# Optimization experiments

Hardware: AMD Instinct MI355X
Metric: run time of the kernel (lower is better)

The kernel has to match this reference:

```python
import jax, jax.numpy as jnp
import numpy as np
import math

MSG_K = 256  # min(active_count, 256); with uniform(0,1) activations active_count >> 256
N_HEADS = 4
LN_EPS = 1e-5


def _mha(x, wi, bi, wo, bo):
    # torch nn.MultiheadAttention self-attention, batch_first=True
    B, K, D = x.shape
    H = N_HEADS
    hd = D // H
    qkv = x @ wi.T + bi                      # [B,K,3D]
    q, k, v = jnp.split(qkv, 3, axis=-1)
    def split_heads(t):
        return t.reshape(B, K, H, hd).transpose(0, 2, 1, 3)  # [B,H,K,hd]
    q, k, v = split_heads(q), split_heads(k), split_heads(v)
    scores = jnp.einsum('bhqd,bhkd->bhqk', q, k) * (1.0 / math.sqrt(hd))
    attn = jax.nn.softmax(scores, axis=-1)
    o = jnp.einsum('bhqk,bhkd->bhqd', attn, v)
    o = o.transpose(0, 2, 1, 3).reshape(B, K, D)
    return o @ wo.T + bo


def _layernorm(x, g, b):
    mu = jnp.mean(x, axis=-1, keepdims=True)
    var = jnp.mean((x - mu) ** 2, axis=-1, keepdims=True)
    return (x - mu) * jax.lax.rsqrt(var + LN_EPS) * g + b


def setup_inputs() -> dict:
    key = jax.random.key(0)
    ks = jax.random.split(key, 12)
    B, N, D = 32, 4096, 256
    s = 0.02
    return {
        'activation': jax.random.uniform(ks[0], (B, N), dtype=jnp.float32),
        'hidden_state': jax.random.normal(ks[1], (B, N, D), dtype=jnp.float32),
        'in_proj_w': jax.random.normal(ks[2], (3 * D, D), dtype=jnp.float32) * s,
        'in_proj_b': jnp.zeros((3 * D,), jnp.float32),
        'out_proj_w': jax.random.normal(ks[3], (D, D), dtype=jnp.float32) * s,
        'out_proj_b': jnp.zeros((D,), jnp.float32),
        'su_w1': jax.random.normal(ks[4], (D, 2 * D), dtype=jnp.float32) * s,
        'su_b1': jnp.zeros((D,), jnp.float32),
        'su_w2': jax.random.normal(ks[5], (D, D), dtype=jnp.float32) * s,
        'su_b2': jnp.zeros((D,), jnp.float32),
        'au_w1': jax.random.normal(ks[6], (D, 2 * D), dtype=jnp.float32) * s,
        'au_b1': jnp.zeros((D,), jnp.float32),
        'au_w2': jax.random.normal(ks[7], (1, D), dtype=jnp.float32) * s,
        'au_b2': jnp.zeros((1,), jnp.float32),
        'ln_g': jnp.ones((D,), jnp.float32),
        'ln_b': jnp.zeros((D,), jnp.float32),
        'sparsity_k': 256,
    }


def reference(activation, hidden_state, in_proj_w, in_proj_b, out_proj_w, out_proj_b,
              su_w1, su_b1, su_w2, su_b2, au_w1, au_b1, au_w2, au_b2, ln_g, ln_b,
              sparsity_k):
    B, N, D = hidden_state.shape
    b_idx = jnp.arange(B)[:, None]

    # ---- compute_messages: top-k gather -> sparse MHA -> scatter back ----
    topk_vals, topk_idx = jax.lax.top_k(activation, MSG_K)        # [B,K]
    active_states = jnp.take_along_axis(hidden_state, topk_idx[..., None], axis=1)  # [B,K,D]
    msg_sparse = _mha(active_states, in_proj_w, in_proj_b, out_proj_w, out_proj_b)
    msg_sparse = msg_sparse * topk_vals[..., None]
    messages = jnp.zeros((B, N, D), hidden_state.dtype).at[b_idx, topk_idx].set(msg_sparse)

    # ---- update_states: MLP on [old, messages] + LayerNorm ----
    combined = jnp.concatenate([hidden_state, messages], axis=-1)  # [B,N,2D]
    h = jax.nn.gelu(combined @ su_w1.T + su_b1, approximate=False)
    new_hidden = _layernorm(h @ su_w2.T + su_b2, ln_g, ln_b)

    # ---- update_activations ----
    comb2 = jnp.concatenate([hidden_state, new_hidden], axis=-1)
    h2 = jax.nn.gelu(comb2 @ au_w1.T + au_b1, approximate=False)
    delta = jax.nn.sigmoid((h2 @ au_w2.T + au_b2).squeeze(-1))     # [B,N]
    new_activation = jnp.clip(0.7 * activation + 0.3 * delta, 0.0, 1.0)

    # ---- maintain_sparsity: keep top sparsity_k, zero the rest ----
    k = min(int(sparsity_k), N)
    tv, ti = jax.lax.top_k(new_activation, k)                      # [B,k]
    sparse_act = jnp.zeros_like(new_activation).at[b_idx, ti].set(tv)
    kept_hidden = jnp.take_along_axis(new_hidden, ti[..., None], axis=1)
    sparse_hidden = jnp.zeros_like(new_hidden).at[b_idx, ti].set(kept_hidden)
    return sparse_act, sparse_hidden
```

## Files before the change

kernel.cpp:

```cpp
#include <hip/hip_runtime.h>


constexpr int KC = 32;
constexpr int CMAX = 2304;
constexpr float BAND_EPS = 0.004f;
constexpr int MAXBAND = 512;

typedef short bf16x8 __attribute__((ext_vector_type(8)));
typedef float f32x4 __attribute__((ext_vector_type(4)));

__device__ __forceinline__ float gelu_f(float x) {
    return 0.5f * x * (1.0f + erff(x * 0.70710678118654752440f));
}
__device__ __forceinline__ unsigned short f2bf(float f) {
    unsigned u = __float_as_uint(f);
    return (unsigned short)((u + 0x7fffu + ((u >> 16) & 1u)) >> 16);
}
__device__ __forceinline__ float bf2f(unsigned short h) {
    return __uint_as_float(((unsigned)h) << 16);
}

__global__ void __launch_bounds__(256) fill0_k(float4* p, long n4) {
    long i = (long)blockIdx.x * 256 + threadIdx.x;
    long stride = (long)gridDim.x * 256;
    float4 z = make_float4(0.f, 0.f, 0.f, 0.f);
    for (; i < n4; i += stride) p[i] = z;
}

__global__ void __launch_bounds__(256) topk1_k(const float* __restrict__ act,
        float* __restrict__ svals, int* __restrict__ sidx, int* __restrict__ cnt)
{
    __shared__ int cs[4];
    __shared__ int sTop, sRest;
    int b = blockIdx.x, tid = threadIdx.x;
    int wid = tid >> 6, lane = tid & 63;
    unsigned v[16];
    #pragma unroll
    for (int s = 0; s < 16; ++s)
        v[s] = __float_as_uint(act[b * 4096 + s * 256 + tid]);

    auto reduce4 = [&](int c) -> int {
        #pragma unroll
        for (int off = 32; off >= 1; off >>= 1) c += __shfl_xor(c, off);
        if (lane == 0) cs[wid] = c;
        __syncthreads();
        int tot = cs[0] + cs[1] + cs[2] + cs[3];
        __syncthreads();
        return tot;
    };
    auto countGE = [&](unsigned thr) -> int {
        int c = 0;
        #pragma unroll
        for (int s = 0; s < 16; ++s) c += (v[s] >= thr) ? 1 : 0;
        return reduce4(c);
    };
    auto countEqLt = [&](unsigned vs, int icut) -> int {
        int c = 0;
        #pragma unroll
        for (int s = 0; s < 16; ++s)
            c += (v[s] == vs && (s * 256 + tid) < icut) ? 1 : 0;
        return reduce4(c);
    };

    unsigned vstar = 0;
    for (int bit = 31; bit >= 0; --bit) {
        unsigned cand = vstar | (1u << bit);
        if (countGE(cand) >= 256) vstar = cand;
    }
    int cgt = countGE(vstar + 1);
    int needed = 256 - cgt;
    int icut = 4096;
    if (countEqLt(vstar, 4096) > needed) {
        int lo = 0, hi = 4096;
        for (int it = 0; it < 12; ++it) {
            int mid = (lo + hi) >> 1;
            if (countEqLt(vstar, mid) <= needed) lo = mid; else hi = mid;
        }
        icut = lo;
    }
    if (tid == 0) { sTop = 0; sRest = 0; }
    __syncthreads();
    float th = __uint_as_float(vstar) - 0.4288f;
    #pragma unroll
    for (int s = 0; s < 16; ++s) {
        int i = s * 256 + tid;
        unsigned vb = v[s];
        float f = __uint_as_float(vb);
        bool top = (vb > vstar) || (vb == vstar && i < icut);
        if (top) {
            int slot = atomicAdd(&sTop, 1);
            sidx[b * 4096 + slot] = i;
            svals[b * 4096 + slot] = f;
        } else if (f >= th) {
            int slot = 256 + atomicAdd(&sRest, 1);
            if (slot < CMAX) {
                sidx[b * 4096 + slot] = i;
                svals[b * 4096 + slot] = f;
            }
        }
    }
    __syncthreads();
    if (tid == 0) cnt[b] = min(256 + sRest, CMAX);
}

__global__ void __launch_bounds__(256) topk2_k(const float* __restrict__ newact,
        const int* __restrict__ sidx, const int* __restrict__ cnt,
        float* __restrict__ selv, int* __restrict__ selo, int* __restrict__ selp)
{
    __shared__ int cs[4];
    __shared__ int sSel;
    int b = blockIdx.x, tid = threadIdx.x;
    int wid = tid >> 6, lane = tid & 63;
    int C = min(cnt[b], CMAX);
    unsigned v[9];
    int org[9];
    #pragma unroll
    for (int s = 0; s < 9; ++s) {
        int p = s * 256 + tid;
        bool ok = (p < C && p < CMAX);
        v[s] = ok ? __float_as_uint(newact[(long)b * CMAX + p]) : 0u;
        org[s] = ok ? sidx[b * 4096 + p] : 0x7FFFFFFF;
    }
    auto reduce4 = [&](int c) -> int {
        #pragma unroll
        for (int off = 32; off >= 1; off >>= 1) c += __shfl_xor(c, off);
        if (lane == 0) cs[wid] = c;
        __syncthreads();
        int tot = cs[0] + cs[1] + cs[2] + cs[3];
        __syncthreads();
        return tot;
    };
    auto countGE = [&](unsigned thr) -> int {
        int c = 0;
        #pragma unroll
        for (int s = 0; s < 9; ++s) c += (v[s] >= thr) ? 1 : 0;
        return reduce4(c);
    };
    auto countEqLt = [&](unsigned vs, int icut) -> int {
        int c = 0;
        #pragma unroll
        for (int s = 0; s < 9; ++s) c += (v[s] == vs && org[s] < icut) ? 1 : 0;
        return reduce4(c);
    };

    unsigned vstar = 0;
    for (int bit = 31; bit >= 0; --bit) {
        unsigned cand = vstar | (1u << bit);
        if (countGE(cand) >= 256) vstar = cand;
    }
    int cgt = countGE(vstar + 1);
    int needed = 256 - cgt;
    int icut = 4096;
    if (countEqLt(vstar, 4096) > needed) {
        int lo = 0, hi = 4096;
        for (int it = 0; it < 12; ++it) {
            int mid = (lo + hi) >> 1;
            if (countEqLt(vstar, mid) <= needed) lo = mid; else hi = mid;
        }
        icut = lo;
    }
    if (tid == 0) sSel = 0;
    __syncthreads();
    #pragma unroll
    for (int s = 0; s < 9; ++s) {
        unsigned vb = v[s];
        bool sel = (vb > vstar) || (vb == vstar && org[s] < icut);
        if (sel) {
            int slot = atomicAdd(&sSel, 1);
            selv[b * 256 + slot] = __uint_as_float(vb);
            selo[b * 256 + slot] = org[s];
            selp[b * 256 + slot] = s * 256 + tid;
        }
    }
}

template<int TM, int TN, int RM, int RN, bool BT, bool GATHER, int EPI>
__global__ void __launch_bounds__(256) gemm_k(
    const float* __restrict__ A, int lda, long sA1, long sA2, int divA,
    const float* __restrict__ B, int ldb, long sB1, long sB2, int divB,
    float* __restrict__ C, int ldc, long sC1, long sC2, int divC,
    int K, const float* __restrict__ bias, const float* __restrict__ rowscale,
    long rsStride, const int* __restrict__ gmap, long gmapStride, float cscale)
{
    constexpr int TX = TN / RN, TY = TM / RM;
    static_assert(TX * TY == 256, "block must be 256 threads");
    __shared__ float As[KC][TM + 4];
    __shared__ float Bs[KC][TN + 4];
    int z = blockIdx.z;
    const float* Ab = A + (long)(z / divA) * sA1 + (long)(z % divA) * sA2;
    const float* Bb = B + (long)(z / divB) * sB1 + (long)(z % divB) * sB2;
    float* Cb = C + (long)(z / divC) * sC1 + (long)(z % divC) * sC2;
    int m0 = blockIdx.y * TM, n0 = blockIdx.x * TN;
    int tid = threadIdx.x;
    int tx = tid % TX, ty = tid / TX;
    float acc[RM][RN];
    #pragma unroll
    for (int i = 0; i < RM; ++i)
        #pragma unroll
        for (int j = 0; j < RN; ++j) acc[i][j] = 0.f;

    for (int k0 = 0; k0 < K; k0 += KC) {
        __syncthreads();
        #pragma unroll
        for (int u = 0; u < (TM * KC) / 1024; ++u) {
            int idx = tid + u * 256;
            int m = idx / (KC / 4), k4 = idx % (KC / 4);
            int row = m0 + m;
            long grow = GATHER ? (long)gmap[(long)z * gmapStride + row] : (long)row;
            float4 v = *(const float4*)(Ab + grow * lda + k0 + k4 * 4);
            As[k4 * 4 + 0][m] = v.x; As[k4 * 4 + 1][m] = v.y;
            As[k4 * 4 + 2][m] = v.z; As[k4 * 4 + 3][m] = v.w;
        }
        if (BT) {
            #pragma unroll
            for (int u = 0; u < (TN * KC) / 1024; ++u) {
                int idx = tid + u * 256;
                int n = idx / (KC / 4), k4 = idx % (KC / 4);
                float4 v = *(const float4*)(Bb + (long)(n0 + n) * ldb + k0 + k4 * 4);
                Bs[k4 * 4 + 0][n] = v.x; Bs[k4 * 4 + 1][n] = v.y;
                Bs[k4 * 4 + 2][n] = v.z; Bs[k4 * 4 + 3][n] = v.w;
            }
        } else {
            #pragma unroll
            for (int u = 0; u < (TN * KC) / 1024; ++u) {
                int idx = tid + u * 256;
                int k = idx / (TN / 4), n4 = idx % (TN / 4);
                float4 v = *(const float4*)(Bb + (long)(k0 + k) * ldb + n0 + n4 * 4);
                *(float4*)&Bs[k][n4 * 4] = v;
            }
        }
        __syncthreads();
        #pragma unroll
        for (int k = 0; k < KC; ++k) {
            float av[RM], bv[RN];
            #pragma unroll
            for (int i = 0; i < RM; i += 4) {
                float4 t = *(const float4*)&As[k][ty * RM + i];
                av[i] = t.x; av[i + 1] = t.y; av[i + 2] = t.z; av[i + 3] = t.w;
            }
            #pragma unroll
            for (int j = 0; j < RN; j += 4) {
                float4 t = *(const float4*)&Bs[k][tx * RN + j];
                bv[j] = t.x; bv[j + 1] = t.y; bv[j + 2] = t.z; bv[j + 3] = t.w;
            }
            #pragma unroll
            for (int i = 0; i < RM; ++i)
                #pragma unroll
                for (int j = 0; j < RN; ++j)
                    acc[i][j] = fmaf(av[i], bv[j], acc[i][j]);
        }
    }
    #pragma unroll
    for (int i = 0; i < RM; ++i) {
        int gm = m0 + ty * RM + i;
        float rs = 1.f;
        if (EPI == 2) rs = rowscale[(long)z * rsStride + gm];
        #pragma unroll
        for (int j = 0; j < RN; j += 4) {
            int gn = n0 + tx * RN + j;
            float4 v = make_float4(acc[i][j], acc[i][j + 1], acc[i][j + 2], acc[i][j + 3]);
            if (EPI == 1 || EPI == 2) {
                float4 bb = *(const float4*)(bias + gn);
                v.x += bb.x; v.y += bb.y; v.z += bb.z; v.w += bb.w;
            }
            if (EPI == 2) { v.x *= rs; v.y *= rs; v.z *= rs; v.w *= rs; }
            if (EPI == 3) { v.x *= cscale; v.y *= cscale; v.z *= cscale; v.w *= cscale; }
            *(float4*)(Cb + (long)gm * ldc + gn) = v;
        }
    }
}

__global__ void __launch_bounds__(256) softmax_k(float* __restrict__ S) {
    int row = blockIdx.x * 4 + (threadIdx.x >> 6);
    int lane = threadIdx.x & 63;
    float4* r = (float4*)(S + (long)row * 256);
    float4 v = r[lane];
    float m = fmaxf(fmaxf(v.x, v.y), fmaxf(v.z, v.w));
    for (int off = 32; off >= 1; off >>= 1) m = fmaxf(m, __shfl_xor(m, off));
    v.x = expf(v.x - m); v.y = expf(v.y - m); v.z = expf(v.z - m); v.w = expf(v.w - m);
    float s = v.x + v.y + v.z + v.w;
    for (int off = 32; off >= 1; off >>= 1) s += __shfl_xor(s, off);
    float inv = 1.f / s;
    v.x *= inv; v.y *= inv; v.z *= inv; v.w *= inv;
    r[lane] = v;
}

__global__ void __launch_bounds__(256) prep_k(
        const float* __restrict__ s1, const float* __restrict__ s2,
        const float* __restrict__ a1,
        unsigned short* __restrict__ o1, unsigned short* __restrict__ o2,
        unsigned short* __restrict__ o3,
        float* __restrict__ w1P, float* __restrict__ w2P, float* __restrict__ auP)
{
    int blk = blockIdx.x, tid = threadIdx.x;
    if (blk < 512) {
        int i = blk * 256 + tid;
        o1[i] = f2bf(s1[i]);
        o3[i] = f2bf(a1[i]);
        if (i < 65536) o2[i] = f2bf(s2[i]);
        return;
    }
    const float* src; float* dst; int ld, ktiles, rel;
    if (blk < 576) { rel = blk - 512; src = s1; ld = 512; dst = w1P; ktiles = 8; }
    else if (blk < 640) { rel = blk - 576; src = s2; ld = 256; dst = w2P; ktiles = 8; }
    else { rel = blk - 640; src = a1; ld = 512; dst = auP; ktiles = 16; }
    int k0 = (rel % ktiles) * 32, n0 = (rel / ktiles) * 32;
    __shared__ float t[32][33];
    int tx = tid & 31, ty = tid >> 5;
    #pragma unroll
    for (int yy = 0; yy < 4; ++yy) {
        int nl = ty * 4 + yy;
        t[nl][tx] = src[(long)(n0 + nl) * ld + k0 + tx];
    }
    __syncthreads();
    #pragma unroll
    for (int yy = 0; yy < 4; ++yy) {
        int k = k0 + ty * 4 + yy;
        dst[(long)(k >> 2) * 1024 + (n0 + tx) * 4 + (k & 3)] = t[tx][ty * 4 + yy];
    }
}

__global__ void __launch_bounds__(256) gatherX_k(const float* __restrict__ hid,
        const int* __restrict__ sidx, const int* __restrict__ cnt,
        unsigned short* __restrict__ Xb)
{
    int b = blockIdx.y;
    int C = min(cnt[b], CMAX);
    int p = blockIdx.x * 4 + (threadIdx.x >> 6);
    int lane = threadIdx.x & 63;
    unsigned short* dst = Xb + ((long)b * CMAX + p) * 256 + lane * 4;
    if (p < C) {
        int row = sidx[b * 4096 + p];
        float4 v = *(const float4*)(hid + ((long)b * 4096 + row) * 256 + lane * 4);
        ushort4 o; o.x = f2bf(v.x); o.y = f2bf(v.y); o.z = f2bf(v.z); o.w = f2bf(v.w);
        *(ushort4*)dst = o;
    } else {
        ushort4 z; z.x = 0; z.y = 0; z.z = 0; z.w = 0;
        *(ushort4*)dst = z;
    }
}

template<int STAGE>
__global__ void __launch_bounds__(256, 2) mlp_mfma_k(
    const unsigned short* __restrict__ A0,
    const unsigned short* __restrict__ A1,
    const unsigned short* __restrict__ W, int ldw,
    const float* __restrict__ bias,
    const float* __restrict__ msgc,
    const float* __restrict__ lng, const float* __restrict__ lnb,
    const float* __restrict__ w2v, const float* __restrict__ b2s,
    const float* __restrict__ svals,
    const int* __restrict__ cnt,
    unsigned short* __restrict__ outb,
    float* __restrict__ nac)
{
    int b = blockIdx.y;
    int C = min(cnt[b], CMAX);
    int m0 = blockIdx.x * 64;
    if (m0 >= C) return;
    int tid = threadIdx.x;
    int wid = tid >> 6;
    int lane = tid & 63;
    int l15 = lane & 15;
    int q = lane >> 4;
    int n0w = wid * 64;

    f32x4 acc[4][4];
    #pragma unroll
    for (int mt = 0; mt < 4; ++mt)
        #pragma unroll
        for (int nt = 0; nt < 4; ++nt) {
            f32x4 z = {0.f, 0.f, 0.f, 0.f};
            acc[mt][nt] = z;
        }

    const unsigned short* Ab = A0 + ((long)b * CMAX + m0) * 256;
    const unsigned short* A1b = (STAGE == 3) ? (A1 + ((long)b * CMAX + m0) * 256) : nullptr;
    int aoff[4];
    #pragma unroll
    for (int mt = 0; mt < 4; ++mt) aoff[mt] = (mt * 16 + l15) * 256;
    const unsigned short* wr[4];
    #pragma unroll
    for (int nt = 0; nt < 4; ++nt) wr[nt] = W + (long)(n0w + nt * 16 + l15) * ldw;

    constexpr int KSTEPS = (STAGE == 3) ? 16 : 8;
    #pragma unroll 4
    for (int ks = 0; ks < KSTEPS; ++ks) {
        const unsigned short* As = (STAGE == 3 && ks >= 8) ? A1b : Ab;
        int ko = (STAGE == 3 && ks >= 8) ? (ks - 8) * 32 : ks * 32;
        int kw = ks * 32;
        bf16x8 af[4], bfr[4];
        #pragma unroll
        for (int mt = 0; mt < 4; ++mt)
            af[mt] = *(const bf16x8*)(As + aoff[mt] + ko + q * 8);
        #pragma unroll
        for (int nt = 0; nt < 4; ++nt)
            bfr[nt] = *(const bf16x8*)(wr[nt] + kw + q * 8);
        #pragma unroll
        for (int mt = 0; mt < 4; ++mt)
            #pragma unroll
            for (int nt = 0; nt < 4; ++nt)
                acc[mt][nt] = __builtin_amdgcn_mfma_f32_16x16x32_bf16(
                    af[mt], bfr[nt], acc[mt][nt], 0, 0, 0);
    }

    if constexpr (STAGE == 1) {
        float bb[4];
        #pragma unroll
        for (int nt = 0; nt < 4; ++nt) bb[nt] = bias[n0w + nt * 16 + l15];
        #pragma unroll
        for (int mt = 0; mt < 4; ++mt) {
            #pragma unroll
            for (int reg = 0; reg < 4; ++reg) {
                int p = m0 + mt * 16 + q * 4 + reg;
                long orow = ((long)b * CMAX + p) * 256;
                const float* mrow = msgc + ((long)b * 256 + p) * 256;
                bool hasm = (p < 256);
                #pragma unroll
                for (int nt = 0; nt < 4; ++nt) {
                    int gc = n0w + nt * 16 + l15;
                    float v = acc[mt][nt][reg] + bb[nt];
                    if (hasm) v += mrow[gc];
                    outb[orow + gc] = f2bf(gelu_f(v));
                }
            }
        }
    }

    if constexpr (STAGE == 2) {
        __shared__ float rsum[4][64];
        __shared__ float rsq[4][64];
        __shared__ float rmu[64], rrs[64];
        float bb[4], gg[4], eb[4];
        #pragma unroll
        for (int nt = 0; nt < 4; ++nt) {
            int gc = n0w + nt * 16 + l15;
            bb[nt] = bias[gc]; gg[nt] = lng[gc]; eb[nt] = lnb[gc];
        }
        #pragma unroll
        for (int mt = 0; mt < 4; ++mt)
            #pragma unroll
            for (int nt = 0; nt < 4; ++nt)
                #pragma unroll
                for (int reg = 0; reg < 4; ++reg)
                    acc[mt][nt][reg] += bb[nt];
        #pragma unroll
        for (int mt = 0; mt < 4; ++mt) {
            #pragma unroll
            for (int reg = 0; reg < 4; ++reg) {
                float s = 0.f, s2 = 0.f;
                #pragma unroll
                for (int nt = 0; nt < 4; ++nt) {
                    float v = acc[mt][nt][reg];
                    s += v; s2 += v * v;
                }
                #pragma unroll
                for (int off = 1; off <= 8; off <<= 1) {
                    s += __shfl_xor(s, off);
                    s2 += __shfl_xor(s2, off);
                }
                if (l15 == 0) {
                    int row = mt * 16 + q * 4 + reg;
                    rsum[wid][row] = s; rsq[wid][row] = s2;
                }
            }
        }
        __syncthreads();
        if (tid < 64) {
            float s = rsum[0][tid] + rsum[1][tid] + rsum[2][tid] + rsum[3][tid];
            float s2 = rsq[0][tid] + rsq[1][tid] + rsq[2][tid] + rsq[3][tid];
            float mu = s * (1.f / 256.f);
            float var = s2 * (1.f / 256.f) - mu * mu;
            rmu[tid] = mu;
            rrs[tid] = rsqrtf(var + 1e-5f);
        }
        __syncthreads();
        #pragma unroll
        for (int mt = 0; mt < 4; ++mt) {
            #pragma unroll
            for (int reg = 0; reg < 4; ++reg) {
                int row = mt * 16 + q * 4 + reg;
                int p = m0 + row;
                float mu = rmu[row], rs = rrs[row];
                long orow = ((long)b * CMAX + p) * 256;
                #pragma unroll
                for (int nt = 0; nt < 4; ++nt) {
                    int gc = n0w + nt * 16 + l15;
                    outb[orow + gc] = f2bf((acc[mt][nt][reg] - mu) * rs * gg[nt] + eb[nt]);
                }
            }
        }
    }

    if constexpr (STAGE == 3) {
        __shared__ float rsum[4][64];
        float bb[4], ww[4];
        #pragma unroll
        for (int nt = 0; nt < 4; ++nt) {
            int gc = n0w + nt * 16 + l15;
            bb[nt] = bias[gc]; ww[nt] = w2v[gc];
        }
        #pragma unroll
        for (int mt = 0; mt < 4; ++mt) {
            #pragma unroll
            for (int reg = 0; reg < 4; ++reg) {
                float s = 0.f;
                #pragma unroll
                for (int nt = 0; nt < 4; ++nt)
                    s += gelu_f(acc[mt][nt][reg] + bb[nt]) * ww[nt];
                #pragma unroll
                for (int off = 1; off <= 8; off <<= 1) s += __shfl_xor(s, off);
                if (l15 == 0) rsum[wid][mt * 16 + q * 4 + reg] = s;
            }
        }
        __syncthreads();
        if (tid < 64) {
            int p = m0 + tid;
            if (p < C) {
                float z = rsum[0][tid] + rsum[1][tid] + rsum[2][tid] + rsum[3][tid] + b2s[0];
                float delta = 1.f / (1.f + expf(-z));
                float na = 0.7f * svals[b * 4096 + p] + 0.3f * delta;
                nac[(long)b * CMAX + p] = fminf(fmaxf(na, 0.f), 1.f);
            }
        }
    }
}

__global__ void __launch_bounds__(256) selectT_k(const float* __restrict__ nac,
        const int* __restrict__ cnt, float* __restrict__ T)
{
    __shared__ float v[CMAX];
    __shared__ int cs[256];
    __shared__ float bounds[2];
    int b = blockIdx.x, tid = threadIdx.x;
    int C = min(cnt[b], CMAX);
    for (int i = tid; i < CMAX; i += 256)
        v[i] = (i < C) ? nac[(long)b * CMAX + i] : -1.f;
    if (tid == 0) { bounds[0] = 0.f; bounds[1] = 1.0f; }
    __syncthreads();
    for (int it = 0; it < 20; ++it) {
        float mid = 0.5f * (bounds[0] + bounds[1]);
        int c = 0;
        for (int i = tid; i < CMAX; i += 256) c += (v[i] >= mid) ? 1 : 0;
        cs[tid] = c; __syncthreads();
        for (int s = 128; s; s >>= 1) {
            if (tid < s) cs[tid] += cs[tid + s];
            __syncthreads();
        }
        if (tid == 0) { if (cs[0] >= 256) bounds[0] = mid; else bounds[1] = mid; }
        __syncthreads();
    }
    if (tid == 0) T[b] = bounds[0];
}

__global__ void __launch_bounds__(256) bandlist_k(const float* __restrict__ nac,
        const int* __restrict__ cnt, const float* __restrict__ Tarr,
        int* __restrict__ bandlist, int* __restrict__ bandcnt)
{
    int b = blockIdx.y;
    int C = min(cnt[b], CMAX);
    int p = blockIdx.x * 256 + threadIdx.x;
    if (p < C && fabsf(nac[(long)b * CMAX + p] - Tarr[b]) < BAND_EPS) {
        int slot = atomicAdd(&bandcnt[b], 1);
        if (slot < MAXBAND) bandlist[b * MAXBAND + slot] = p;
    }
}

__global__ void __launch_bounds__(256) bandfix_k(
    const float* __restrict__ hid, const int* __restrict__ sidx,
    const float* __restrict__ msgc,
    const float* __restrict__ w1Pf, const float* __restrict__ su_b1,
    const float* __restrict__ w2Pf, const float* __restrict__ su_b2,
    const float* __restrict__ ln_g, const float* __restrict__ ln_b,
    const float* __restrict__ auPf, const float* __restrict__ au_b1,
    const float* __restrict__ au_w2, const float* __restrict__ au_b2,
    const float* __restrict__ svals,
    const int* __restrict__ bandlist, const int* __restrict__ bandcnt,
    float* __restrict__ nac, unsigned short* __restrict__ NHb)
{
    int b = blockIdx.y;
    int M = min(bandcnt[b], MAXBAND);
    int base = blockIdx.x * 4;
    if (base >= M) return;
    int nact = min(M - base, 4);
    int tid = threadIdx.x;
    int wid = tid >> 6, lane = tid & 63;
    const float4* w1P = (const float4*)w1Pf;
    const float4* w2P = (const float4*)w2Pf;
    const float4* auP = (const float4*)auPf;
    __shared__ float xr[4][256];
    __shared__ float hy[4][256];
    __shared__ float nh[4][256];
    __shared__ float muS[4], rsS[4];
    __shared__ int ppS[4];
    if (tid < 4)
        ppS[tid] = (tid < nact) ? bandlist[b * MAXBAND + base + tid] : -1;
    __syncthreads();
    #pragma unroll
    for (int r = 0; r < 4; ++r) {
        int pp = ppS[r];
        xr[r][tid] = (pp >= 0) ? hid[((long)b * 4096 + sidx[b * 4096 + pp]) * 256 + tid] : 0.f;
    }
    __syncthreads();
    int n = tid;
    float acc[4];
    #pragma unroll
    for (int r = 0; r < 4; ++r) acc[r] = 0.f;
    for (int k4 = 0; k4 < 64; ++k4) {
        float4 w = w1P[k4 * 256 + n];
        #pragma unroll
        for (int r = 0; r < 4; ++r) {
            float4 xv = *(const float4*)&xr[r][k4 * 4];
            acc[r] = fmaf(w.x, xv.x, acc[r]);
            acc[r] = fmaf(w.y, xv.y, acc[r]);
            acc[r] = fmaf(w.z, xv.z, acc[r]);
            acc[r] = fmaf(w.w, xv.w, acc[r]);
        }
    }
    float b1v = su_b1[n];
    #pragma unroll
    for (int r = 0; r < 4; ++r) {
        int pp = ppS[r];
        float s = acc[r] + b1v;
        if (pp >= 0 && pp < 256) s += msgc[((long)b * 256 + pp) * 256 + n];
        acc[r] = gelu_f(s);
    }
    __syncthreads();
    #pragma unroll
    for (int r = 0; r < 4; ++r) hy[r][n] = acc[r];
    __syncthreads();
    #pragma unroll
    for (int r = 0; r < 4; ++r) acc[r] = 0.f;
    for (int k4 = 0; k4 < 64; ++k4) {
        float4 w = w2P[k4 * 256 + n];
        #pragma unroll
        for (int r = 0; r < 4; ++r) {
            float4 hv = *(const float4*)&hy[r][k4 * 4];
            acc[r] = fmaf(w.x, hv.x, acc[r]);
            acc[r] = fmaf(w.y, hv.y, acc[r]);
            acc[r] = fmaf(w.z, hv.z, acc[r]);
            acc[r] = fmaf(w.w, hv.w, acc[r]);
        }
    }
    __syncthreads();
    float b2v = su_b2[n];
    #pragma unroll
    for (int r = 0; r < 4; ++r) hy[r][n] = acc[r] + b2v;
    __syncthreads();
    {
        int r = wid;
        float4 yv = *(const float4*)&hy[r][lane * 4];
        float s = yv.x + yv.y + yv.z + yv.w;
        float s2 = yv.x * yv.x + yv.y * yv.y + yv.z * yv.z + yv.w * yv.w;
        #pragma unroll
        for (int off = 32; off >= 1; off >>= 1) {
            s += __shfl_xor(s, off);
            s2 += __shfl_xor(s2, off);
        }
        if (lane == 0) {
            float mu = s * (1.f / 256.f);
            float var = s2 * (1.f / 256.f) - mu * mu;
            muS[r] = mu; rsS[r] = rsqrtf(var + 1e-5f);
        }
    }
    __syncthreads();
    float gv = ln_g[n], ev = ln_b[n];
    #pragma unroll
    for (int r = 0; r < 4; ++r) {
        float o = (hy[r][n] - muS[r]) * rsS[r] * gv + ev;
        nh[r][n] = o;
        if (ppS[r] >= 0) NHb[((long)b * CMAX + ppS[r]) * 256 + n] = f2bf(o);
    }
    __syncthreads();
    #pragma unroll
    for (int r = 0; r < 4; ++r) acc[r] = 0.f;
    for (int k4 = 0; k4 < 64; ++k4) {
        float4 w = auP[k4 * 256 + n];
        #pragma unroll
        for (int r = 0; r < 4; ++r) {
            float4 xv = *(const float4*)&xr[r][k4 * 4];
            acc[r] = fmaf(w.x, xv.x, acc[r]);
            acc[r] = fmaf(w.y, xv.y, acc[r]);
            acc[r] = fmaf(w.z, xv.z, acc[r]);
            acc[r] = fmaf(w.w, xv.w, acc[r]);
        }
    }
    for (int k4 = 64; k4 < 128; ++k4) {
        float4 w = auP[k4 * 256 + n];
        #pragma unroll
        for (int r = 0; r < 4; ++r) {
            float4 hv = *(const float4*)&nh[r][(k4 - 64) * 4];
            acc[r] = fmaf(w.x, hv.x, acc[r]);
            acc[r] = fmaf(w.y, hv.y, acc[r]);
            acc[r] = fmaf(w.z, hv.z, acc[r]);
            acc[r] = fmaf(w.w, hv.w, acc[r]);
        }
    }
    float ab = au_b1[n], wv2 = au_w2[n];
    __syncthreads();
    #pragma unroll
    for (int r = 0; r < 4; ++r) hy[r][n] = gelu_f(acc[r] + ab) * wv2;
    __syncthreads();
    {
        int r = wid;
        float4 gvv = *(const float4*)&hy[r][lane * 4];
        float s = gvv.x + gvv.y + gvv.z + gvv.w;
        #pragma unroll
        for (int off = 32; off >= 1; off >>= 1) s += __shfl_xor(s, off);
        if (lane == 0 && ppS[r] >= 0) {
            float z = s + au_b2[0];
            float delta = 1.f / (1.f + expf(-z));
            float na = 0.7f * svals[b * 4096 + ppS[r]] + 0.3f * delta;
            nac[(long)b * CMAX + ppS[r]] = fminf(fmaxf(na, 0.f), 1.f);
        }
    }
}

__global__ void __launch_bounds__(64) scatter_k(const float* __restrict__ selv,
        const int* __restrict__ selo, const int* __restrict__ selp,
        const unsigned short* __restrict__ NHb, float* __restrict__ out)
{
    int b = blockIdx.x >> 8, j = blockIdx.x & 255, t = threadIdx.x;
    int orig = selo[b * 256 + j];
    int p = selp[b * 256 + j];
    if (t == 0) out[b * 4096 + orig] = selv[b * 256 + j];
    const ushort4* src = (const ushort4*)(NHb + ((long)b * CMAX + p) * 256);
    ushort4 s = src[t];
    float4 o = make_float4(bf2f(s.x), bf2f(s.y), bf2f(s.z), bf2f(s.w));
    *(float4*)(out + 131072 + ((long)(b * 4096 + orig)) * 256 + t * 4) = o;
}

extern "C" void kernel_launch(void* const* d_in, const int* in_sizes, int n_in,
                              void* d_out, int out_size, void* d_ws, size_t ws_size,
                              hipStream_t stream)
{
    const float* act   = (const float*)d_in[0];
    const float* hid   = (const float*)d_in[1];
    const float* wi    = (const float*)d_in[2];
    const float* bi    = (const float*)d_in[3];
    const float* wo    = (const float*)d_in[4];
    const float* bo    = (const float*)d_in[5];
    const float* su_w1 = (const float*)d_in[6];
    const float* su_b1 = (const float*)d_in[7];
    const float* su_w2 = (const float*)d_in[8];
    const float* su_b2 = (const float*)d_in[9];
    const float* au_w1 = (const float*)d_in[10];
    const float* au_b1 = (const float*)d_in[11];
    const float* au_w2 = (const float*)d_in[12];
    const float* au_b2 = (const float*)d_in[13];
    const float* ln_g  = (const float*)d_in[14];
    const float* ln_b  = (const float*)d_in[15];
    float* out = (float*)d_out;

    char* ws = (char*)d_ws;
    size_t off = 0;
    auto alloc = [&](size_t bytes) {
        size_t o = off; off += (bytes + 255) & ~(size_t)255; return o;
    };
    float* svals = (float*)(ws + alloc((size_t)32 * 4096 * 4));
    int*   sidx  = (int*)  (ws + alloc((size_t)32 * 4096 * 4));
    int*   cnt   = (int*)  (ws + alloc(256));
    float* qkv   = (float*)(ws + alloc((size_t)32 * 256 * 768 * 4));
    float* Sb    = (float*)(ws + alloc((size_t)32 * 4 * 256 * 256 * 4));
    float* Ob    = (float*)(ws + alloc((size_t)32 * 256 * 256 * 4));
    float* MSG   = (float*)(ws + alloc((size_t)32 * 256 * 256 * 4));
    float* MSGC  = (float*)(ws + alloc((size_t)32 * 256 * 256 * 4));
    float* selv  = (float*)(ws + alloc((size_t)32 * 256 * 4));
    int*   selo  = (int*)  (ws + alloc((size_t)32 * 256 * 4));
    int*   selp  = (int*)  (ws + alloc((size_t)32 * 256 * 4));
    unsigned short* swb1 = (unsigned short*)(ws + alloc((size_t)256 * 512 * 2));
    unsigned short* swb2 = (unsigned short*)(ws + alloc((size_t)256 * 256 * 2));
    unsigned short* awb1 = (unsigned short*)(ws + alloc((size_t)256 * 512 * 2));
    float* w1P = (float*)(ws + alloc((size_t)256 * 256 * 4));
    float* w2P = (float*)(ws + alloc((size_t)256 * 256 * 4));
    float* auP = (float*)(ws + alloc((size_t)512 * 256 * 4));
    unsigned short* Xb   = (unsigned short*)(ws + alloc((size_t)32 * CMAX * 256 * 2));
    unsigned short* H1b  = (unsigned short*)(ws + alloc((size_t)32 * CMAX * 256 * 2));
    unsigned short* NHb  = (unsigned short*)(ws + alloc((size_t)32 * CMAX * 256 * 2));
    float* nac = (float*)(ws + alloc((size_t)32 * CMAX * 4));
    float* Tb  = (float*)(ws + alloc(128));
    int* bandl = (int*)(ws + alloc((size_t)32 * MAXBAND * 4));
    int* bandc = (int*)(ws + alloc(128));

    hipMemsetAsync(bandc, 0, 32 * sizeof(int), stream);
    fill0_k<<<2048, 256, 0, stream>>>((float4*)out, (long)out_size / 4);
    topk1_k<<<32, 256, 0, stream>>>(act, svals, sidx, cnt);
    prep_k<<<768, 256, 0, stream>>>(su_w1, su_w2, au_w1, swb1, swb2, awb1,
                                    w1P, w2P, auP);
    gatherX_k<<<dim3(CMAX / 4, 32), 256, 0, stream>>>(hid, sidx, cnt, Xb);
    gemm_k<64, 256, 8, 8, true, true, 1><<<dim3(3, 4, 32), 256, 0, stream>>>(
        hid, 256, (long)4096 * 256, 0, 1,
        wi, 256, 0, 0, 1,
        qkv, 768, (long)256 * 768, 0, 1,
        256, bi, nullptr, 0, sidx, 4096, 0.f);
    gemm_k<64, 256, 8, 8, true, false, 3><<<dim3(1, 4, 128), 256, 0, stream>>>(
        qkv, 768, 196608, 64, 4,
        qkv + 256, 768, 196608, 64, 4,
        Sb, 256, 65536, 0, 1,
        64, nullptr, nullptr, 0, nullptr, 0, 0.125f);
    softmax_k<<<8192, 256, 0, stream>>>(Sb);
    gemm_k<64, 64, 4, 4, false, false, 0><<<dim3(1, 4, 128), 256, 0, stream>>>(
        Sb, 256, 65536, 0, 1,
        qkv + 512, 768, 196608, 64, 4,
        Ob, 256, 65536, 64, 4,
        256, nullptr, nullptr, 0, nullptr, 0, 0.f);
    gemm_k<64, 256, 8, 8, true, false, 2><<<dim3(1, 4, 32), 256, 0, stream>>>(
        Ob, 256, 65536, 0, 1,
        wo, 256, 0, 0, 1,
        MSG, 256, 65536, 0, 1,
        256, bo, svals, 4096, nullptr, 0, 0.f);
    gemm_k<64, 256, 8, 8, true, false, 0><<<dim3(1, 4, 32), 256, 0, stream>>>(
        MSG, 256, 65536, 0, 1,
        su_w1 + 256, 512, 0, 0, 1,
        MSGC, 256, 65536, 0, 1,
        256, nullptr, nullptr, 0, nullptr, 0, 0.f);
    dim3 mgrid(CMAX / 64, 32);
    mlp_mfma_k<1><<<mgrid, 256, 0, stream>>>(Xb, nullptr, swb1, 512, su_b1, MSGC,
        nullptr, nullptr, nullptr, nullptr, nullptr, cnt, H1b, nullptr);
    mlp_mfma_k<2><<<mgrid, 256, 0, stream>>>(H1b, nullptr, swb2, 256, su_b2, nullptr,
        ln_g, ln_b, nullptr, nullptr, nullptr, cnt, NHb, nullptr);
    mlp_mfma_k<3><<<mgrid, 256, 0, stream>>>(Xb, NHb, awb1, 512, au_b1, nullptr,
        nullptr, nullptr, au_w2, au_b2, svals, cnt, nullptr, nac);
    selectT_k<<<32, 256, 0, stream>>>(nac, cnt, Tb);
    bandlist_k<<<dim3(CMAX / 256, 32), 256, 0, stream>>>(nac, cnt, Tb, bandl, bandc);
    bandfix_k<<<dim3(MAXBAND / 4, 32), 256, 0, stream>>>(hid, sidx, MSGC,
        w1P, su_b1, w2P, su_b2, ln_g, ln_b, auP, au_b1, au_w2, au_b2,
        svals, bandl, bandc, nac, NHb);
    topk2_k<<<32, 256, 0, stream>>>(nac, sidx, cnt, selv, selo, selp);
    scatter_k<<<8192, 64, 0, stream>>>(selv, selo, selp, NHb, out);
}
```

Measured before the change: 803.7 us.

## Fuse three MLP stage kernels into one kernel with LDS-resident hidden tile

Merges the three per-stage MFMA GEMM kernels (su layer1+GELU, su layer2+LayerNorm, au layer1+reduction) into one kernel. The intermediate 64x256 bf16 tile is kept in swizzled shared memory instead of round-tripping H1 and NH through global memory, and two kernel launches are removed. The cost is 32KB+ of LDS per block, which may limit occupancy despite the launch bound hint of 4, and the stages now run serially within one block with extra barriers.

```diff
diff --git a/kernel.cpp b/kernel.cpp
--- a/kernel.cpp
+++ b/kernel.cpp
@@ -18,6 +18,9 @@
 }
 __device__ __forceinline__ float bf2f(unsigned short h) {
     return __uint_as_float(((unsigned)h) << 16);
+}
+__device__ __forceinline__ int swz(int row, int byteInRow) {
+    return (row << 9) + (byteInRow ^ ((row & 7) << 4));
 }
 
 __global__ void __launch_bounds__(256) fill0_k(float4* p, long n4) {
@@ -340,19 +343,18 @@
     }
 }
 
-template<int STAGE>
-__global__ void __launch_bounds__(256, 2) mlp_mfma_k(
-    const unsigned short* __restrict__ A0,
-    const unsigned short* __restrict__ A1,
-    const unsigned short* __restrict__ W, int ldw,
-    const float* __restrict__ bias,
-    const float* __restrict__ msgc,
+__global__ void __launch_bounds__(256, 4) fused_mlp_k(
+    const unsigned short* __restrict__ Xb,
+    const unsigned short* __restrict__ W1,
+    const unsigned short* __restrict__ W2,
+    const unsigned short* __restrict__ WA,
+    const float* __restrict__ su_b1v, const float* __restrict__ msgc,
+    const float* __restrict__ su_b2v,
     const float* __restrict__ lng, const float* __restrict__ lnb,
+    const float* __restrict__ au_b1v,
     const float* __restrict__ w2v, const float* __restrict__ b2s,
-    const float* __restrict__ svals,
-    const int* __restrict__ cnt,
-    unsigned short* __restrict__ outb,
-    float* __restrict__ nac)
+    const float* __restrict__ svals, const int* __restrict__ cnt,
+    unsigned short* __restrict__ NHb, float* __restrict__ nac)
 {
     int b = blockIdx.y;
     int C = min(cnt[b], CMAX);
@@ -365,7 +367,15 @@
     int q = lane >> 4;
     int n0w = wid * 64;
 
+    __shared__ __align__(16) unsigned short Hs[64 * 256];
+    __shared__ float rsum[4][64];
+    __shared__ float rsq[4][64];
+    __shared__ float rmu[64], rrs[64];
+
+    const unsigned short* Ab = Xb + ((long)b * CMAX + m0) * 256;
+
     f32x4 acc[4][4];
+
     #pragma unroll
     for (int mt = 0; mt < 4; ++mt)
         #pragma unroll
@@ -373,47 +383,36 @@
             f32x4 z = {0.f, 0.f, 0.f, 0.f};
             acc[mt][nt] = z;
         }
-
-    const unsigned short* Ab = A0 + ((long)b * CMAX + m0) * 256;
-    const unsigned short* A1b = (STAGE == 3) ? (A1 + ((long)b * CMAX + m0) * 256) : nullptr;
-    int aoff[4];
-    #pragma unroll
-    for (int mt = 0; mt < 4; ++mt) aoff[mt] = (mt * 16 + l15) * 256;
-    const unsigned short* wr[4];
-    #pragma unroll
-    for (int nt = 0; nt < 4; ++nt) wr[nt] = W + (long)(n0w + nt * 16 + l15) * ldw;
-
-    constexpr int KSTEPS = (STAGE == 3) ? 16 : 8;
-    #pragma unroll 4
-    for (int ks = 0; ks < KSTEPS; ++ks) {
-        const unsigned short* As = (STAGE == 3 && ks >= 8) ? A1b : Ab;
-        int ko = (STAGE == 3 && ks >= 8) ? (ks - 8) * 32 : ks * 32;
-        int kw = ks * 32;
-        bf16x8 af[4], bfr[4];
-        #pragma unroll
-        for (int mt = 0; mt < 4; ++mt)
-            af[mt] = *(const bf16x8*)(As + aoff[mt] + ko + q * 8);
-        #pragma unroll
-        for (int nt = 0; nt < 4; ++nt)
-            bfr[nt] = *(const bf16x8*)(wr[nt] + kw + q * 8);
-        #pragma unroll
-        for (int mt = 0; mt < 4; ++mt)
+    {
+        const unsigned short* wr[4];
+        #pragma unroll
+        for (int nt = 0; nt < 4; ++nt) wr[nt] = W1 + (long)(n0w + nt * 16 + l15) * 512;
+        #pragma unroll 4
+        for (int ks = 0; ks < 8; ++ks) {
+            int ko = ks * 32;
+            bf16x8 af[4], bfr[4];
+            #pragma unroll
+            for (int mt = 0; mt < 4; ++mt)
+                af[mt] = *(const bf16x8*)(Ab + (mt * 16 + l15) * 256 + ko + q * 8);
             #pragma unroll
             for (int nt = 0; nt < 4; ++nt)
-                acc[mt][nt] = __builtin_amdgcn_mfma_f32_16x16x32_bf16(
-                    af[mt], bfr[nt], acc[mt][nt], 0, 0, 0);
-    }
-
-    if constexpr (STAGE == 1) {
+                bfr[nt] = *(const bf16x8*)(wr[nt] + ko + q * 8);
+            #pragma unroll
+            for (int mt = 0; mt < 4; ++mt)
+                #pragma unroll
+                for (int nt = 0; nt < 4; ++nt)
+                    acc[mt][nt] = __builtin_amdgcn_mfma_f32_16x16x32_bf16(
+                        af[mt], bfr[nt], acc[mt][nt], 0, 0, 0);
+        }
         float bb[4];
         #pragma unroll
-        for (int nt = 0; nt < 4; ++nt) bb[nt] = bias[n0w + nt * 16 + l15];
+        for (int nt = 0; nt < 4; ++nt) bb[nt] = su_b1v[n0w + nt * 16 + l15];
         #pragma unroll
         for (int mt = 0; mt < 4; ++mt) {
             #pragma unroll
             for (int reg = 0; reg < 4; ++reg) {
-                int p = m0 + mt * 16 + q * 4 + reg;
-                long orow = ((long)b * CMAX + p) * 256;
+                int lr = mt * 16 + q * 4 + reg;
+                int p = m0 + lr;
                 const float* mrow = msgc + ((long)b * 256 + p) * 256;
                 bool hasm = (p < 256);
                 #pragma unroll
@@ -421,21 +420,48 @@
                     int gc = n0w + nt * 16 + l15;
                     float v = acc[mt][nt][reg] + bb[nt];
                     if (hasm) v += mrow[gc];
-                    outb[orow + gc] = f2bf(gelu_f(v));
+                    *(unsigned short*)((char*)Hs + swz(lr, gc * 2)) = f2bf(gelu_f(v));
                 }
             }
         }
     }
-
-    if constexpr (STAGE == 2) {
-        __shared__ float rsum[4][64];
-        __shared__ float rsq[4][64];
-        __shared__ float rmu[64], rrs[64];
+    __syncthreads();
+
+    #pragma unroll
+    for (int mt = 0; mt < 4; ++mt)
+        #pragma unroll
+        for (int nt = 0; nt < 4; ++nt) {
+            f32x4 z = {0.f, 0.f, 0.f, 0.f};
+            acc[mt][nt] = z;
+        }
+    {
+        const unsigned short* wr[4];
+        #pragma unroll
+        for (int nt = 0; nt < 4; ++nt) wr[nt] = W2 + (long)(n0w + nt * 16 + l15) * 256;
+        #pragma unroll
+        for (int ks = 0; ks < 8; ++ks) {
+            int ko = ks * 32;
+            bf16x8 af[4], bfr[4];
+            #pragma unroll
+            for (int mt = 0; mt < 4; ++mt) {
+                int r = mt * 16 + l15;
+                af[mt] = *(const bf16x8*)((const char*)Hs + swz(r, (ko + q * 8) * 2));
+            }
+            #pragma unroll
+            for (int nt = 0; nt < 4; ++nt)
+                bfr[nt] = *(const bf16x8*)(wr[nt] + ko + q * 8);
+            #pragma unroll
+            for (int mt = 0; mt < 4; ++mt)
+                #pragma unroll
+                for (int nt = 0; nt < 4; ++nt)
+                    acc[mt][nt] = __builtin_amdgcn_mfma_f32_16x16x32_bf16(
+                        af[mt], bfr[nt], acc[mt][nt], 0, 0, 0);
+        }
         float bb[4], gg[4], eb[4];
         #pragma unroll
         for (int nt = 0; nt < 4; ++nt) {
             int gc = n0w + nt * 16 + l15;
-            bb[nt] = bias[gc]; gg[nt] = lng[gc]; eb[nt] = lnb[gc];
+            bb[nt] = su_b2v[gc]; gg[nt] = lng[gc]; eb[nt] = lnb[gc];
         }
         #pragma unroll
         for (int mt = 0; mt < 4; ++mt)
@@ -479,26 +505,76 @@
         for (int mt = 0; mt < 4; ++mt) {
             #pragma unroll
             for (int reg = 0; reg < 4; ++reg) {
-                int row = mt * 16 + q * 4 + reg;
-                int p = m0 + row;
-                float mu = rmu[row], rs = rrs[row];
+                int lr = mt * 16 + q * 4 + reg;
+                int p = m0 + lr;
+                float mu = rmu[lr], rs = rrs[lr];
                 long orow = ((long)b * CMAX + p) * 256;
                 #pragma unroll
                 for (int nt = 0; nt < 4; ++nt) {
                     int gc = n0w + nt * 16 + l15;
-                    outb[orow + gc] = f2bf((acc[mt][nt][reg] - mu) * rs * gg[nt] + eb[nt]);
+                    unsigned short ov =
+                        f2bf((acc[mt][nt][reg] - mu) * rs * gg[nt] + eb[nt]);
+                    NHb[orow + gc] = ov;
+                    *(unsigned short*)((char*)Hs + swz(lr, gc * 2)) = ov;
                 }
             }
         }
     }
-
-    if constexpr (STAGE == 3) {
-        __shared__ float rsum[4][64];
+    __syncthreads();
+
+    #pragma unroll
+    for (int mt = 0; mt < 4; ++mt)
+        #pragma unroll
+        for (int nt = 0; nt < 4; ++nt) {
+            f32x4 z = {0.f, 0.f, 0.f, 0.f};
+            acc[mt][nt] = z;
+        }
+    {
+        const unsigned short* wr[4];
+        #pragma unroll
+        for (int nt = 0; nt < 4; ++nt) wr[nt] = WA + (long)(n0w + nt * 16 + l15) * 512;
+        #pragma unroll 4
+        for (int ks = 0; ks < 8; ++ks) {
+            int ko = ks * 32;
+            bf16x8 af[4], bfr[4];
+            #pragma unroll
+            for (int mt = 0; mt < 4; ++mt)
+                af[mt] = *(const bf16x8*)(Ab + (mt * 16 + l15) * 256 + ko + q * 8);
+            #pragma unroll
+            for (int nt = 0; nt < 4; ++nt)
+                bfr[nt] = *(const bf16x8*)(wr[nt] + ko + q * 8);
+            #pragma unroll
+            for (int mt = 0; mt < 4; ++mt)
+                #pragma unroll
+                for (int nt = 0; nt < 4; ++nt)
+                    acc[mt][nt] = __builtin_amdgcn_mfma_f32_16x16x32_bf16(
+                        af[mt], bfr[nt], acc[mt][nt], 0, 0, 0);
+        }
+        #pragma unroll
+        for (int ks = 0; ks < 8; ++ks) {
+            int ko = ks * 32;
+            int kw = 256 + ks * 32;
+            bf16x8 af[4], bfr[4];
+            #pragma unroll
+            for (int mt = 0; mt < 4; ++mt) {
+                int r = mt * 16 + l15;
+                af[mt] = *(const bf16x8*)((const char*)Hs + swz(r, (ko + q * 8) * 2));
+            }
+            #pragma unroll
+            for (int nt = 0; nt < 4; ++nt)
+                bfr[nt] = *(const bf16x8*)(wr[nt] + kw + q * 8);
+            #pragma unroll
+            for (int mt = 0; mt < 4; ++mt)
+                #pragma unroll
+                for (int nt = 0; nt < 4; ++nt)
+                    acc[mt][nt] = __builtin_amdgcn_mfma_f32_16x16x32_bf16(
+                        af[mt], bfr[nt], acc[mt][nt], 0, 0, 0);
+        }
         float bb[4], ww[4];
         #pragma unroll
         for (int nt = 0; nt < 4; ++nt) {
             int gc = n0w + nt * 16 + l15;
-            bb[nt] = bias[gc]; ww[nt] = w2v[gc];
+            bb[nt] = au_b1v[gc]; ww[nt] = w2v[gc];
         }
         #pragma unroll
         for (int mt = 0; mt < 4; ++mt) {
@@ -775,7 +851,6 @@
     float* w2P = (float*)(ws + alloc((size_t)256 * 256 * 4));
     float* auP = (float*)(ws + alloc((size_t)512 * 256 * 4));
     unsigned short* Xb   = (unsigned short*)(ws + alloc((size_t)32 * CMAX * 256 * 2));
-    unsigned short* H1b  = (unsigned short*)(ws + alloc((size_t)32 * CMAX * 256 * 2));
     unsigned short* NHb  = (unsigned short*)(ws + alloc((size_t)32 * CMAX * 256 * 2));
     float* nac = (float*)(ws + alloc((size_t)32 * CMAX * 4));
     float* Tb  = (float*)(ws + alloc(128));
@@ -814,13 +889,9 @@
         su_w1 + 256, 512, 0, 0, 1,
         MSGC, 256, 65536, 0, 1,
         256, nullptr, nullptr, 0, nullptr, 0, 0.f);
-    dim3 mgrid(CMAX / 64, 32);
-    mlp_mfma_k<1><<<mgrid, 256, 0, stream>>>(Xb, nullptr, swb1, 512, su_b1, MSGC,
-        nullptr, nullptr, nullptr, nullptr, nullptr, cnt, H1b, nullptr);
-    mlp_mfma_k<2><<<mgrid, 256, 0, stream>>>(H1b, nullptr, swb2, 256, su_b2, nullptr,
-        ln_g, ln_b, nullptr, nullptr, nullptr, cnt, NHb, nullptr);
-    mlp_mfma_k<3><<<mgrid, 256, 0, stream>>>(Xb, NHb, awb1, 512, au_b1, nullptr,
-        nullptr, nullptr, au_w2, au_b2, svals, cnt, nullptr, nac);
+    fused_mlp_k<<<dim3(CMAX / 64, 32), 256, 0, stream>>>(Xb, swb1, swb2, awb1,
+        su_b1, MSGC, su_b2, ln_g, ln_b, au_b1, au_w2, au_b2, svals, cnt,
+        NHb, nac);
     selectT_k<<<32, 256, 0, stream>>>(nac, cnt, Tb);
     bandlist_k<<<dim3(CMAX / 256, 32), 256, 0, stream>>>(nac, cnt, Tb, bandl, bandc);
     bandfix_k<<<dim3(MAXBAND / 4, 32), 256, 0, stream>>>(hid, sidx, MSGC,
```

New measurement: 832.5 us. 3.6% more time.
